# Performance work log

Hardware: AMD Instinct MI355X
Metric: run time of the kernel (lower is better)

Reference implementation:

```python
import jax, jax.numpy as jnp
import numpy as np

OUT_FEATURES = 11008
IN_FEATURES = 4096
BLOCK_SIZE = 128
NUM_BLOCKS = IN_FEATURES // BLOCK_SIZE  # 32
M_TOKENS = 4096  # flattened batch*seq


def _pack_int4(q):
    # q: int8 values in [-8, 7], flattened; pack 2 nibbles per int8 (matches pack_int4_to_int8)
    flat = q.reshape(-1)
    u = (flat.astype(jnp.int32) + 8).astype(jnp.uint8)
    packed = (u[0::2] | (u[1::2] << 4)).astype(jnp.int8)
    return packed


def _unpack_int4(packed, shape):
    # matches unpack_int8_to_int4
    pu = packed.astype(jnp.uint8)
    lower = pu & 15
    upper = (pu >> 4) & 15
    un = jnp.stack([lower, upper], axis=1).reshape(-1)
    n = int(np.prod(shape))
    un = un[:n].astype(jnp.int8) - 8
    return un.reshape(shape)


def setup_inputs() -> dict:
    key = jax.random.key(0)
    k_x, k_w, k_b = jax.random.split(key, 3)
    x = jax.random.normal(k_x, (M_TOKENS, IN_FEATURES), dtype=jnp.float32)
    w = jax.random.normal(k_w, (OUT_FEATURES, IN_FEATURES), dtype=jnp.float32) * 0.02
    bias = jax.random.normal(k_b, (OUT_FEATURES,), dtype=jnp.float32) * 0.01
    # blockwise symmetric 4-bit quantization (matches _quantize_blockwise)
    wr = w.reshape(OUT_FEATURES, NUM_BLOCKS, BLOCK_SIZE).transpose(1, 2, 0)  # (nb, bs, out)
    max_val = jnp.max(jnp.abs(wr), axis=1, keepdims=True)  # (nb, 1, out)
    qmax = 7.0
    scale3 = jnp.clip(max_val / qmax, 1e-8, None)
    q = jnp.clip(jnp.round(wr / scale3), -8, 7).astype(jnp.int8)  # (nb, bs, out)
    scale = scale3.squeeze(1)  # (nb, out)
    packed_w = _pack_int4(q)
    return {"x": x, "packed_w": packed_w, "scale": scale, "bias": bias}


def reference(x, packed_w, scale, bias):
    # unpack int4 nibbles -> (num_blocks, block_size, out)
    q = _unpack_int4(packed_w, (NUM_BLOCKS, BLOCK_SIZE, OUT_FEATURES))
    # dequantize with per-(block, out-channel) scale
    w_deq = q.astype(jnp.float32) * scale[:, None, :]  # (nb, bs, out)
    # y = x @ W^T + b, with x blocked along the in dimension
    xb = x.reshape(x.shape[0], NUM_BLOCKS, BLOCK_SIZE)
    y = jnp.einsum('mnb,nbo->mo', xb, w_deq) + bias
    return y
```

## Files before the change

### kernel.cpp

```cpp
#include <hip/hip_runtime.h>
#include <hip/hip_bf16.h>
#include <stdint.h>

#define NOUT 11008
#define KIN  4096
#define MTOK 4096
#define PLD  5504
#define BM 256
#define BN 128
#define BK 32
#define NSTEP (KIN/BK)
#define NTN (NOUT/BN)
#define NTM (MTOK/BM)
#define ACHUNK 16384
#define WSA_BYTES ((size_t)NTM * NSTEP * ACHUNK)
#define WSB_OFF   WSA_BYTES

typedef short bf16x8 __attribute__((ext_vector_type(8)));
typedef float f32x4  __attribute__((ext_vector_type(4)));

typedef __attribute__((address_space(3))) uint8_t lds_u8_t;
typedef __attribute__((address_space(1))) const uint8_t glb_u8_t;

__device__ __forceinline__ uint32_t bfpack(float lo, float hi){
    __hip_bfloat16 a = __float2bfloat16(lo);
    __hip_bfloat16 b = __float2bfloat16(hi);
    uint16_t ua, ub;
    __builtin_memcpy(&ua, &a, 2);
    __builtin_memcpy(&ub, &b, 2);
    return (uint32_t)ua | ((uint32_t)ub << 16);
}

__device__ __forceinline__ int swzA(int m){ return ((m >> 1) & 3) << 4; }

__global__ __launch_bounds__(256)
void prepA(const float* __restrict__ x, uint8_t* __restrict__ wsA)
{
    int gid = blockIdx.x * 256 + threadIdx.x;
    int m  = gid >> 10;
    int k  = (gid & 1023) << 2;
    float4 v = *reinterpret_cast<const float4*>(x + (size_t)m * KIN + k);
    uint32_t lo = bfpack(v.x, v.y), hi = bfpack(v.z, v.w);
    int mt = m >> 8, ml = m & 255, t = k >> 5, kl = k & 31;
    size_t dst = (size_t)(mt * NSTEP + t) * ACHUNK + ml * 64 + ((kl * 2) ^ swzA(ml));
    *reinterpret_cast<uint2*>(wsA + dst) = make_uint2(lo, hi);
}

__global__ __launch_bounds__(128)
void prepB(const int32_t* __restrict__ pw, uint8_t* __restrict__ wsB)
{
    int np   = blockIdx.x * 128 + threadIdx.x;
    int koct = blockIdx.y;
    const int32_t* p = pw + (size_t)koct * 8 * PLD + np;
    uint32_t b[8];
#pragma unroll
    for (int i = 0; i < 8; ++i) b[i] = (uint32_t)p[(size_t)i * PLD] & 0xFFu;
    uint32_t lo = b[0] | (b[1] << 8) | (b[2] << 16) | (b[3] << 24);
    uint32_t hi = b[4] | (b[5] << 8) | (b[6] << 16) | (b[7] << 24);
    *reinterpret_cast<uint2*>(wsB + ((size_t)koct * PLD + np) * 8) = make_uint2(lo, hi);
}

__global__ __launch_bounds__(256, 2)
void qlin_gemm(const uint8_t* __restrict__ wsA, const uint8_t* __restrict__ wsB,
               const float* __restrict__ sc, const float* __restrict__ bias,
               float* __restrict__ y)
{
    __shared__ __align__(16) uint8_t ldsA[3][BM * 64];
    __shared__ __align__(16) uint8_t ldsB[3][64 * 128];

    const int tid  = threadIdx.x;
    const int lane = tid & 63;
    const int wid  = tid >> 6;
    const int wr = wid >> 1, wc = wid & 1;

    const int lb = (blockIdx.x & 7) * 172 + (blockIdx.x >> 3);
    const int mt = lb / NTN, nt = lb % NTN;
    const int m0 = mt * BM, n0 = nt * BN;

    const int cl = lane & 15;
    const int k8 = lane >> 4;

    int aOff[8];
#pragma unroll
    for (int i = 0; i < 8; ++i) {
        int ml = wr * 128 + i * 16 + cl;
        aOff[i] = ml * 64 + ((k8 * 16) ^ swzA(ml));
    }
    int bOff[4][2];
#pragma unroll
    for (int j = 0; j < 4; ++j) {
        int n = wc * 64 + j * 16 + cl;
        int npr = n >> 1, p = n & 1;
#pragma unroll
        for (int h = 0; h < 2; ++h) {
            int q8 = k8 * 2 + h;
            bOff[j][h] = npr * 128 + (((q8 ^ (npr & 7)) << 4)) + (((p ^ ((npr >> 3) & 1)) << 3));
        }
    }
    const int npw  = tid & 63;
    const int koct = wid;
    const int sww  = (npw >> 3) & 1;
    int wOff[2][2];
#pragma unroll
    for (int kq = 0; kq < 2; ++kq)
#pragma unroll
        for (int p = 0; p < 2; ++p)
            wOff[kq][p] = npw * 128 + ((((koct * 2 + kq) ^ (npw & 7)) << 4)) + (((p ^ sww) << 3));

    const size_t npg = (size_t)(n0 >> 1) + npw;
    const uint8_t* wsAbase = wsA + (size_t)mt * NSTEP * ACHUNK;
    const float* scb = sc + n0 + 2 * npw;

    f32x4 acc[8][4];
#pragma unroll
    for (int i = 0; i < 8; ++i)
#pragma unroll
        for (int j = 0; j < 4; ++j)
            acc[i][j] = (f32x4){0.f, 0.f, 0.f, 0.f};

    auto issueA = [&](int t, int buf) {
        const uint8_t* g = wsAbase + (size_t)t * ACHUNK + tid * 16;
        lds_u8_t* l = (lds_u8_t*)(&ldsA[buf][tid * 16]);
#pragma unroll
        for (int q = 0; q < 4; ++q)
            __builtin_amdgcn_global_load_lds((glb_u8_t*)(g + q * 4096), l + q * 4096, 16, 0, 0);
    };
    auto loadB = [&](int t) {
        return *reinterpret_cast<const uint2*>(wsB + ((size_t)(t * 4 + koct) * PLD + npg) * 8);
    };
    auto loadS = [&](int t) {
        return *reinterpret_cast<const float2*>(scb + (size_t)(t >> 2) * NOUT);
    };
    auto decodeWrite = [&](uint2 braw, float2 s, int buf) {
        uint8_t* Lb = ldsB[buf];
        const float a0 = -8.f * s.x, a1 = -8.f * s.y;
        uint32_t l0 = braw.x & 0x0F0F0F0Fu, h0 = (braw.x >> 4) & 0x0F0F0F0Fu;
        uint32_t l1 = braw.y & 0x0F0F0F0Fu, h1 = (braw.y >> 4) & 0x0F0F0F0Fu;
        float fe[8], fo[8];
#pragma unroll
        for (int i = 0; i < 4; ++i) {
            fe[i]     = fmaf((float)((l0 >> (8 * i)) & 0xFFu), s.x, a0);
            fe[i + 4] = fmaf((float)((l1 >> (8 * i)) & 0xFFu), s.x, a0);
            fo[i]     = fmaf((float)((h0 >> (8 * i)) & 0xFFu), s.y, a1);
            fo[i + 4] = fmaf((float)((h1 >> (8 * i)) & 0xFFu), s.y, a1);
        }
        uint2 g;
        g.x = bfpack(fe[0], fe[1]); g.y = bfpack(fe[2], fe[3]);
        *reinterpret_cast<uint2*>(Lb + wOff[0][0]) = g;
        g.x = bfpack(fe[4], fe[5]); g.y = bfpack(fe[6], fe[7]);
        *reinterpret_cast<uint2*>(Lb + wOff[1][0]) = g;
        g.x = bfpack(fo[0], fo[1]); g.y = bfpack(fo[2], fo[3]);
        *reinterpret_cast<uint2*>(Lb + wOff[0][1]) = g;
        g.x = bfpack(fo[4], fo[5]); g.y = bfpack(fo[6], fo[7]);
        *reinterpret_cast<uint2*>(Lb + wOff[1][1]) = g;
    };
    auto compute = [&](int buf) {
        const uint8_t* La = ldsA[buf];
        const uint8_t* Lb = ldsB[buf];
        bf16x8 af[8], bfr[4];
#pragma unroll
        for (int i = 0; i < 8; ++i)
            af[i] = *reinterpret_cast<const bf16x8*>(La + aOff[i]);
#pragma unroll
        for (int j = 0; j < 4; ++j) {
            uint64_t v[2];
            v[0] = *reinterpret_cast<const uint64_t*>(Lb + bOff[j][0]);
            v[1] = *reinterpret_cast<const uint64_t*>(Lb + bOff[j][1]);
            __builtin_memcpy(&bfr[j], v, 16);
        }
        __builtin_amdgcn_s_setprio(1);
#pragma unroll
        for (int i = 0; i < 8; ++i)
#pragma unroll
            for (int j = 0; j < 4; ++j)
                acc[i][j] = __builtin_amdgcn_mfma_f32_16x16x32_bf16(af[i], bfr[j], acc[i][j], 0, 0, 0);
        __builtin_amdgcn_s_setprio(0);
    };

    issueA(0, 0);
    asm volatile("" ::: "memory");
    uint2  braw_cur = loadB(0);
    float2 sfl_cur  = loadS(0);
    asm volatile("" ::: "memory");
    issueA(1, 1);
    asm volatile("" ::: "memory");
    uint2  braw_nxt = loadB(1);
    float2 sfl_nxt  = loadS(1);
    asm volatile("" ::: "memory");
    decodeWrite(braw_cur, sfl_cur, 0);
    asm volatile("s_waitcnt vmcnt(6) lgkmcnt(0)" ::: "memory");
    __builtin_amdgcn_sched_barrier(0);
    __builtin_amdgcn_s_barrier();
    asm volatile("" ::: "memory");

    int bc = 0, bw = 1, bi = 2;
#pragma unroll 1
    for (int t = 0; t < NSTEP; ++t) {
        const int tp = (t + 2 < NSTEP) ? (t + 2) : (NSTEP - 1);
        issueA(tp, bi);
        asm volatile("" ::: "memory");
        uint2  braw2 = loadB(tp);
        float2 sfl2  = loadS(tp);
        decodeWrite(braw_nxt, sfl_nxt, bw);
        compute(bc);
        braw_nxt = braw2; sfl_nxt = sfl2;
        asm volatile("s_waitcnt vmcnt(6) lgkmcnt(0)" ::: "memory");
        __builtin_amdgcn_sched_barrier(0);
        __builtin_amdgcn_s_barrier();
        asm volatile("" ::: "memory");
        int nb = bc; bc = bw; bw = bi; bi = nb;
    }

    float bv[4];
#pragma unroll
    for (int j = 0; j < 4; ++j) bv[j] = bias[n0 + wc * 64 + j * 16 + cl];
    const int rg = (lane >> 4) * 4;
#pragma unroll
    for (int i = 0; i < 8; ++i) {
        const int mrow = m0 + wr * 128 + i * 16 + rg;
#pragma unroll
        for (int r = 0; r < 4; ++r) {
            float* yp = y + (size_t)(mrow + r) * NOUT + n0 + wc * 64 + cl;
#pragma unroll
            for (int j = 0; j < 4; ++j)
                yp[j * 16] = acc[i][j][r] + bv[j];
        }
    }
}

extern "C" void kernel_launch(void* const* d_in, const int* in_sizes, int n_in,
                              void* d_out, int out_size, void* d_ws, size_t ws_size,
                              hipStream_t stream)
{
    const float*   xin  = (const float*)d_in[0];
    const int32_t* pw   = (const int32_t*)d_in[1];
    const float*   scal = (const float*)d_in[2];
    const float*   bias = (const float*)d_in[3];
    float* y = (float*)d_out;

    uint8_t* wsA = (uint8_t*)d_ws;
    uint8_t* wsB = wsA + WSB_OFF;

    prepA<<<dim3((MTOK * (KIN / 4)) / 256), 256, 0, stream>>>(xin, wsA);
    prepB<<<dim3(43, 512), 128, 0, stream>>>(pw, wsB);
    qlin_gemm<<<dim3(NTM * NTN), 256, 0, stream>>>(wsA, wsB, scal, bias, y);
}
```

Before: 452.6 us.

## Pre-dequantize weights to swizzled bf16 tiles and stream both operands via LDS DMA

Adds a prep kernel that dequantizes the int4 weights once into bf16 chunks already laid out in the swizzled LDS format. A new GEMM kernel then loads both A and B tiles with global_load_lds, with no per-step register decode or scale loads in the main loop. This removes decode ALU work and register-to-LDS writes from every GEMM tile, which were repeated across the 16 M-tiles. In exchange the GEMM reads 4x more weight bytes and needs extra workspace. The old path is kept as a fallback when the workspace is too small.

```diff
diff --git a/kernel.cpp b/kernel.cpp
--- a/kernel.cpp
+++ b/kernel.cpp
@@ -13,8 +13,11 @@
 #define NTN (NOUT/BN)
 #define NTM (MTOK/BM)
 #define ACHUNK 16384
+#define BCHUNK 8192
 #define WSA_BYTES ((size_t)NTM * NSTEP * ACHUNK)
+#define WSW_BYTES ((size_t)NTN * NSTEP * BCHUNK)
 #define WSB_OFF   WSA_BYTES
+#define WS_NEED_NEW (WSA_BYTES + WSW_BYTES)
 
 typedef short bf16x8 __attribute__((ext_vector_type(8)));
 typedef float f32x4  __attribute__((ext_vector_type(4)));
@@ -46,6 +49,176 @@
     *reinterpret_cast<uint2*>(wsA + dst) = make_uint2(lo, hi);
 }
 
+__global__ __launch_bounds__(256)
+void prepW(const int32_t* __restrict__ pw, const float* __restrict__ sc,
+           uint8_t* __restrict__ wsW)
+{
+    const int t  = blockIdx.x;
+    const int nt = blockIdx.y;
+    const int tid  = threadIdx.x;
+    const int npw  = tid & 63;
+    const int koct = tid >> 6;
+
+    const int kbase = t * BK + koct * 8;
+    const int np    = nt * 64 + npw;
+    const int32_t* p = pw + (size_t)kbase * PLD + np;
+    uint32_t b[8];
+#pragma unroll
+    for (int i = 0; i < 8; ++i) b[i] = (uint32_t)p[(size_t)i * PLD] & 0xFFu;
+
+    const int kb = t >> 2;
+    const float s0 = sc[(size_t)kb * NOUT + 2 * np];
+    const float s1 = sc[(size_t)kb * NOUT + 2 * np + 1];
+    const float a0 = -8.f * s0, a1 = -8.f * s1;
+    float fe[8], fo[8];
+#pragma unroll
+    for (int i = 0; i < 8; ++i) {
+        fe[i] = fmaf((float)(b[i] & 15u), s0, a0);
+        fo[i] = fmaf((float)(b[i] >> 4),  s1, a1);
+    }
+
+    const int sww = (npw >> 3) & 1;
+    uint8_t* out = wsW + (size_t)(nt * NSTEP + t) * BCHUNK;
+    int wOff[2][2];
+#pragma unroll
+    for (int kq = 0; kq < 2; ++kq)
+#pragma unroll
+        for (int pp = 0; pp < 2; ++pp)
+            wOff[kq][pp] = npw * 128 + ((((koct * 2 + kq) ^ (npw & 7)) << 4)) + (((pp ^ sww) << 3));
+
+    uint2 g;
+    g.x = bfpack(fe[0], fe[1]); g.y = bfpack(fe[2], fe[3]);
+    *reinterpret_cast<uint2*>(out + wOff[0][0]) = g;
+    g.x = bfpack(fe[4], fe[5]); g.y = bfpack(fe[6], fe[7]);
+    *reinterpret_cast<uint2*>(out + wOff[1][0]) = g;
+    g.x = bfpack(fo[0], fo[1]); g.y = bfpack(fo[2], fo[3]);
+    *reinterpret_cast<uint2*>(out + wOff[0][1]) = g;
+    g.x = bfpack(fo[4], fo[5]); g.y = bfpack(fo[6], fo[7]);
+    *reinterpret_cast<uint2*>(out + wOff[1][1]) = g;
+}
+
+__global__ __launch_bounds__(256, 2)
+void qlin_gemm_pre(const uint8_t* __restrict__ wsA, const uint8_t* __restrict__ wsW,
+                   const float* __restrict__ bias, float* __restrict__ y)
+{
+    __shared__ __align__(16) uint8_t ldsA[3][ACHUNK];
+    __shared__ __align__(16) uint8_t ldsB[3][BCHUNK];
+
+    const int tid  = threadIdx.x;
+    const int lane = tid & 63;
+    const int wid  = tid >> 6;
+    const int wr = wid >> 1, wc = wid & 1;
+
+    const int lb = (blockIdx.x & 7) * 172 + (blockIdx.x >> 3);
+    const int mt = lb / NTN, nt = lb % NTN;
+    const int m0 = mt * BM, n0 = nt * BN;
+
+    const int cl = lane & 15;
+    const int k8 = lane >> 4;
+
+    int aOff[8];
+#pragma unroll
+    for (int i = 0; i < 8; ++i) {
+        int ml = wr * 128 + i * 16 + cl;
+        aOff[i] = ml * 64 + ((k8 * 16) ^ swzA(ml));
+    }
+    int bOff[4][2];
+#pragma unroll
+    for (int j = 0; j < 4; ++j) {
+        int n = wc * 64 + j * 16 + cl;
+        int npr = n >> 1, p = n & 1;
+#pragma unroll
+        for (int h = 0; h < 2; ++h) {
+            int q8 = k8 * 2 + h;
+            bOff[j][h] = npr * 128 + (((q8 ^ (npr & 7)) << 4)) + (((p ^ ((npr >> 3) & 1)) << 3));
+        }
+    }
+
+    const uint8_t* wsAbase = wsA + (size_t)mt * NSTEP * ACHUNK;
+    const uint8_t* wsWbase = wsW + (size_t)nt * NSTEP * BCHUNK;
+
+    f32x4 acc[8][4];
+#pragma unroll
+    for (int i = 0; i < 8; ++i)
+#pragma unroll
+        for (int j = 0; j < 4; ++j)
+            acc[i][j] = (f32x4){0.f, 0.f, 0.f, 0.f};
+
+    auto issueA = [&](int t, int buf) {
+        const uint8_t* g = wsAbase + (size_t)t * ACHUNK + tid * 16;
+        lds_u8_t* l = (lds_u8_t*)(&ldsA[buf][tid * 16]);
+#pragma unroll
+        for (int q = 0; q < 4; ++q)
+            __builtin_amdgcn_global_load_lds((glb_u8_t*)(g + q * 4096), l + q * 4096, 16, 0, 0);
+    };
+    auto issueB = [&](int t, int buf) {
+        const uint8_t* g = wsWbase + (size_t)t * BCHUNK + tid * 16;
+        lds_u8_t* l = (lds_u8_t*)(&ldsB[buf][tid * 16]);
+        __builtin_amdgcn_global_load_lds((glb_u8_t*)(g),        l,        16, 0, 0);
+        __builtin_amdgcn_global_load_lds((glb_u8_t*)(g + 4096), l + 4096, 16, 0, 0);
+    };
+    auto compute = [&](int buf) {
+        const uint8_t* La = ldsA[buf];
+        const uint8_t* Lb = ldsB[buf];
+        bf16x8 af[8], bfr[4];
+#pragma unroll
+        for (int i = 0; i < 8; ++i)
+            af[i] = *reinterpret_cast<const bf16x8*>(La + aOff[i]);
+#pragma unroll
+        for (int j = 0; j < 4; ++j) {
+            uint64_t v[2];
+            v[0] = *reinterpret_cast<const uint64_t*>(Lb + bOff[j][0]);
+            v[1] = *reinterpret_cast<const uint64_t*>(Lb + bOff[j][1]);
+            __builtin_memcpy(&bfr[j], v, 16);
+        }
+        __builtin_amdgcn_s_setprio(1);
+#pragma unroll
+        for (int i = 0; i < 8; ++i)
+#pragma unroll
+            for (int j = 0; j < 4; ++j)
+                acc[i][j] = __builtin_amdgcn_mfma_f32_16x16x32_bf16(af[i], bfr[j], acc[i][j], 0, 0, 0);
+        __builtin_amdgcn_s_setprio(0);
+    };
+
+    issueA(0, 0); issueB(0, 0);
+    issueA(1, 1); issueB(1, 1);
+    asm volatile("s_waitcnt vmcnt(6)" ::: "memory");
+    __builtin_amdgcn_sched_barrier(0);
+    __builtin_amdgcn_s_barrier();
+    asm volatile("" ::: "memory");
+
+    int bc = 0, bi = 2;
+#pragma unroll 1
+    for (int t = 0; t < NSTEP; ++t) {
+        const int tp = (t + 2 < NSTEP) ? (t + 2) : (NSTEP - 1);
+        issueA(tp, bi);
+        issueB(tp, bi);
+        compute(bc);
+        asm volatile("s_waitcnt vmcnt(6)" ::: "memory");
+        __builtin_amdgcn_sched_barrier(0);
+        __builtin_amdgcn_s_barrier();
+        asm volatile("" ::: "memory");
+        bc = (bc == 2) ? 0 : bc + 1;
+        bi = (bi == 2) ? 0 : bi + 1;
+    }
+
+    float bv[4];
+#pragma unroll
+    for (int j = 0; j < 4; ++j) bv[j] = bias[n0 + wc * 64 + j * 16 + cl];
+    const int rg = (lane >> 4) * 4;
+#pragma unroll
+    for (int i = 0; i < 8; ++i) {
+        const int mrow = m0 + wr * 128 + i * 16 + rg;
+#pragma unroll
+        for (int r = 0; r < 4; ++r) {
+            float* yp = y + (size_t)(mrow + r) * NOUT + n0 + wc * 64 + cl;
+#pragma unroll
+            for (int j = 0; j < 4; ++j)
+                yp[j * 16] = acc[i][j][r] + bv[j];
+        }
+    }
+}
+
 __global__ __launch_bounds__(128)
 void prepB(const int32_t* __restrict__ pw, uint8_t* __restrict__ wsB)
 {
@@ -61,9 +234,9 @@
 }
 
 __global__ __launch_bounds__(256, 2)
-void qlin_gemm(const uint8_t* __restrict__ wsA, const uint8_t* __restrict__ wsB,
-               const float* __restrict__ sc, const float* __restrict__ bias,
-               float* __restrict__ y)
+void qlin_gemm_v5(const uint8_t* __restrict__ wsA, const uint8_t* __restrict__ wsB,
+                  const float* __restrict__ sc, const float* __restrict__ bias,
+                  float* __restrict__ y)
 {
     __shared__ __align__(16) uint8_t ldsA[3][BM * 64];
     __shared__ __align__(16) uint8_t ldsB[3][64 * 128];
@@ -134,8 +307,8 @@
     auto decodeWrite = [&](uint2 braw, float2 s, int buf) {
         uint8_t* Lb = ldsB[buf];
         const float a0 = -8.f * s.x, a1 = -8.f * s.y;
-        uint32_t l0 = braw.x & 0x0F0F0F0Fu, h0 = (braw.x >> 4) & 0x0F0F0F0Fu;
-        uint32_t l1 = braw.y & 0x0F0F0F0Fu, h1 = (braw.y >> 4) & 0x0F0F0F0Fu;
+        uint32_t l0 = braw.x & 0x0f0f0f0fu, h0 = (braw.x >> 4) & 0x0f0f0f0fu;
+        uint32_t l1 = braw.y & 0x0f0f0f0fu, h1 = (braw.y >> 4) & 0x0f0f0f0fu;
         float fe[8], fo[8];
 #pragma unroll
         for (int i = 0; i < 4; ++i) {
@@ -239,9 +412,16 @@
     float* y = (float*)d_out;
 
     uint8_t* wsA = (uint8_t*)d_ws;
-    uint8_t* wsB = wsA + WSB_OFF;
 
     prepA<<<dim3((MTOK * (KIN / 4)) / 256), 256, 0, stream>>>(xin, wsA);
-    prepB<<<dim3(43, 512), 128, 0, stream>>>(pw, wsB);
-    qlin_gemm<<<dim3(NTM * NTN), 256, 0, stream>>>(wsA, wsB, scal, bias, y);
-}
+
+    if (ws_size >= WS_NEED_NEW) {
+        uint8_t* wsW = wsA + WSA_BYTES;
+        prepW<<<dim3(NSTEP, NTN), 256, 0, stream>>>(pw, scal, wsW);
+        qlin_gemm_pre<<<dim3(NTM * NTN), 256, 0, stream>>>(wsA, wsW, bias, y);
+    } else {
+        uint8_t* wsB = wsA + WSB_OFF;
+        prepB<<<dim3(43, 512), 128, 0, stream>>>(pw, wsB);
+        qlin_gemm_v5<<<dim3(NTM * NTN), 256, 0, stream>>>(wsA, wsB, scal, bias, y);
+    }
+}
```

Result: slower. 504.4 us (+11.5%).
